# Optimization experiments

Measured on AMD Instinct MI355X. Metric: run time of the kernel, lower is better.

The kernel has to match this reference:

```python
import jax, jax.numpy as jnp
import numpy as np

TAU_S = 5.0  # network_config['tau_s']; n_steps inferred from trailing dim


def psp(x, tau_s):
    """Leaky synaptic integrator along the last (time) axis.
    x: [B, C, H, W, T] -> syns: [B, C, H, W, T]
    syn_t = syn_{t-1} * (1 - 1/tau_s) + x_t ;  out_t = syn_t / tau_s
    """
    decay = 1.0 - 1.0 / tau_s
    xt = jnp.moveaxis(x, -1, 0)  # [T, B, C, H, W]

    def step(syn, inp):
        syn = syn * decay + inp
        return syn, syn / tau_s

    _, ys = jax.lax.scan(step, jnp.zeros_like(xt[0]), xt)
    return jnp.moveaxis(ys, 0, -1)  # [B, C, H, W, T]


def setup_inputs() -> dict:
    key = jax.random.key(0)
    k1, k2 = jax.random.split(key)
    B, C, H, W, T = 32, 256, 4, 4, 100
    outputs = jax.random.normal(k1, (B, C, H, W, T), dtype=jnp.float32)
    # target is a spike train in the original; uniform [0,1) floats keep the
    # same math and dtype (fill='rand' per input_specs)
    target = jax.random.uniform(k2, (B, C, H, W, T), dtype=jnp.float32)
    return {"outputs": outputs, "target": target}


def reference(outputs, target):
    # spike_kernel: delta = outputs - psp(target); loss = 0.5 * sum(delta^2)
    delta = outputs - psp(target, TAU_S)
    return 0.5 * jnp.sum(delta * delta)
```

## Files before the change

kernel.cpp:

```cpp
#include <hip/hip_runtime.h>


#define BLOCK 256

__global__ __launch_bounds__(BLOCK) void spike_loss_kernel(
    const float4* __restrict__ o4g, const float4* __restrict__ x4g,
    float* __restrict__ out) {
  const int r = blockIdx.x * BLOCK + threadIdx.x;
  const float4* __restrict__ op = o4g + (size_t)r * 25;
  const float4* __restrict__ xp = x4g + (size_t)r * 25;

  float4 xc[5], oc[5], xn[5], on[5];
#pragma unroll
  for (int j = 0; j < 5; ++j) { xc[j] = xp[j]; oc[j] = op[j]; }

  float syn = 0.f;
  float l0 = 0.f, l1 = 0.f, l2 = 0.f, l3 = 0.f;
#pragma unroll
  for (int c = 0; c < 5; ++c) {
    if (c < 4) {
#pragma unroll
      for (int j = 0; j < 5; ++j) {
        xn[j] = xp[(c + 1) * 5 + j];
        on[j] = op[(c + 1) * 5 + j];
      }
    }
#pragma unroll
    for (int j = 0; j < 5; ++j) {
      float a;
      syn = fmaf(0.8f, syn, xc[j].x); a = fmaf(-0.2f, syn, oc[j].x); l0 = fmaf(a, a, l0);
      syn = fmaf(0.8f, syn, xc[j].y); a = fmaf(-0.2f, syn, oc[j].y); l1 = fmaf(a, a, l1);
      syn = fmaf(0.8f, syn, xc[j].z); a = fmaf(-0.2f, syn, oc[j].z); l2 = fmaf(a, a, l2);
      syn = fmaf(0.8f, syn, xc[j].w); a = fmaf(-0.2f, syn, oc[j].w); l3 = fmaf(a, a, l3);
    }
    if (c < 4) {
#pragma unroll
      for (int j = 0; j < 5; ++j) { xc[j] = xn[j]; oc[j] = on[j]; }
    }
  }
  float loss = (l0 + l1) + (l2 + l3);

#pragma unroll
  for (int off = 32; off > 0; off >>= 1) loss += __shfl_down(loss, off, 64);

  __shared__ float wsum[BLOCK / 64];
  const int lane = threadIdx.x & 63;
  const int w    = threadIdx.x >> 6;
  if (lane == 0) wsum[w] = loss;
  __syncthreads();
  if (threadIdx.x == 0) {
    float v = (wsum[0] + wsum[1]) + (wsum[2] + wsum[3]);
    atomicAdd(out, 0.5f * v);
  }
}

extern "C" void kernel_launch(void* const* d_in, const int* in_sizes, int n_in,
                              void* d_out, int out_size, void* d_ws, size_t ws_size,
                              hipStream_t stream) {
  const float4* o4 = (const float4*)d_in[0];
  const float4* x4 = (const float4*)d_in[1];
  float* loss = (float*)d_out;

  const int rows = in_sizes[0] / 100;
  const int grid = rows / BLOCK;

  hipLaunchKernelGGL(spike_loss_kernel, dim3(grid), dim3(BLOCK), 0, stream,
                     o4, x4, loss);
}
```

Baseline: 143.2 us.

## Decompose scan into per-chunk local partials with coalesced loads and LDS carry pass

Each float4 chunk is now processed independently with coalesced loads across the block. Each chunk gets a local 4-step integration assuming zero incoming state, plus the local squared error and a linear term. The carried synaptic state is then reconstructed per row in a second pass over LDS, expanding the squared error algebraically with precomputed decay-power constants. This removes strided per-thread row loads, at the cost of LDS traffic, a block barrier, half the threads idling in the second pass, and a slightly different float rounding order.

Result: faster. 122.7 us (-14.3%).

```diff
diff --git a/kernel.cpp b/kernel.cpp
--- a/kernel.cpp
+++ b/kernel.cpp
@@ -2,53 +2,86 @@
 
 
 #define BLOCK 256
+#define RPB   128
+#define F4PB  (RPB * 25)
+
+constexpr double dpow(double b, int n) {
+  double r = 1.0; for (int i = 0; i < n; ++i) r *= b; return r;
+}
+constexpr float K4  = (float)dpow(0.8, 4);
+constexpr float B0d = (float)(0.4 * dpow(0.8, 1));
+constexpr float B1d = (float)(0.4 * dpow(0.8, 2));
+constexpr float B2d = (float)(0.4 * dpow(0.8, 3));
+constexpr float B3d = (float)(0.4 * dpow(0.8, 4));
+constexpr float G4C = (float)(0.04 * (dpow(0.8, 2) + dpow(0.8, 4) +
+                                      dpow(0.8, 6) + dpow(0.8, 8)));
 
 __global__ __launch_bounds__(BLOCK) void spike_loss_kernel(
     const float4* __restrict__ o4g, const float4* __restrict__ x4g,
     float* __restrict__ out) {
-  const int r = blockIdx.x * BLOCK + threadIdx.x;
-  const float4* __restrict__ op = o4g + (size_t)r * 25;
-  const float4* __restrict__ xp = x4g + (size_t)r * 25;
+  __shared__ float UB[2 * F4PB];
+  __shared__ float wsum[BLOCK / 64];
 
-  float4 xc[5], oc[5], xn[5], on[5];
+  const int t = threadIdx.x;
+  const size_t base = (size_t)blockIdx.x * F4PB;
+  const float4* __restrict__ xp = x4g + base;
+  const float4* __restrict__ op = o4g + base;
+
+  float loss = 0.f;
+
+  float4 xa = xp[t], oa = op[t];
+  int i = t;
 #pragma unroll
-  for (int j = 0; j < 5; ++j) { xc[j] = xp[j]; oc[j] = op[j]; }
+  for (int k = 0; k < 12; ++k) {
+    float4 xb, ob;
+    if ((k < 11) || (t < RPB)) { xb = xp[i + BLOCK]; ob = op[i + BLOCK]; }
+    float u, a, abar, bb;
+    u = xa.x;                 a = fmaf(-0.2f, u, oa.x);
+    abar = a * a;             bb = a * B0d;
+    u = fmaf(0.8f, u, xa.y);  a = fmaf(-0.2f, u, oa.y);
+    abar = fmaf(a, a, abar);  bb = fmaf(a, B1d, bb);
+    u = fmaf(0.8f, u, xa.z);  a = fmaf(-0.2f, u, oa.z);
+    abar = fmaf(a, a, abar);  bb = fmaf(a, B2d, bb);
+    u = fmaf(0.8f, u, xa.w);  a = fmaf(-0.2f, u, oa.w);
+    abar = fmaf(a, a, abar);  bb = fmaf(a, B3d, bb);
+    loss += abar;
+    UB[i] = u; UB[F4PB + i] = bb;
+    xa = xb; oa = ob; i += BLOCK;
+  }
+  if (t < RPB) {
+    float u, a, abar, bb;
+    u = xa.x;                 a = fmaf(-0.2f, u, oa.x);
+    abar = a * a;             bb = a * B0d;
+    u = fmaf(0.8f, u, xa.y);  a = fmaf(-0.2f, u, oa.y);
+    abar = fmaf(a, a, abar);  bb = fmaf(a, B1d, bb);
+    u = fmaf(0.8f, u, xa.z);  a = fmaf(-0.2f, u, oa.z);
+    abar = fmaf(a, a, abar);  bb = fmaf(a, B2d, bb);
+    u = fmaf(0.8f, u, xa.w);  a = fmaf(-0.2f, u, oa.w);
+    abar = fmaf(a, a, abar);  bb = fmaf(a, B3d, bb);
+    loss += abar;
+    UB[i] = u; UB[F4PB + i] = bb;
+  }
+  __syncthreads();
 
-  float syn = 0.f;
-  float l0 = 0.f, l1 = 0.f, l2 = 0.f, l3 = 0.f;
+  if (t < RPB) {
+    float sig = 0.f, l2 = 0.f;
+    const int rb = t * 25;
 #pragma unroll
-  for (int c = 0; c < 5; ++c) {
-    if (c < 4) {
-#pragma unroll
-      for (int j = 0; j < 5; ++j) {
-        xn[j] = xp[(c + 1) * 5 + j];
-        on[j] = op[(c + 1) * 5 + j];
-      }
+    for (int c = 0; c < 25; ++c) {
+      const float u  = UB[rb + c];
+      const float bb = UB[F4PB + rb + c];
+      l2  = fmaf(fmaf(G4C, sig, -bb), sig, l2);
+      sig = fmaf(K4, sig, u);
     }
-#pragma unroll
-    for (int j = 0; j < 5; ++j) {
-      float a;
-      syn = fmaf(0.8f, syn, xc[j].x); a = fmaf(-0.2f, syn, oc[j].x); l0 = fmaf(a, a, l0);
-      syn = fmaf(0.8f, syn, xc[j].y); a = fmaf(-0.2f, syn, oc[j].y); l1 = fmaf(a, a, l1);
-      syn = fmaf(0.8f, syn, xc[j].z); a = fmaf(-0.2f, syn, oc[j].z); l2 = fmaf(a, a, l2);
-      syn = fmaf(0.8f, syn, xc[j].w); a = fmaf(-0.2f, syn, oc[j].w); l3 = fmaf(a, a, l3);
-    }
-    if (c < 4) {
-#pragma unroll
-      for (int j = 0; j < 5; ++j) { xc[j] = xn[j]; oc[j] = on[j]; }
-    }
+    loss += l2;
   }
-  float loss = (l0 + l1) + (l2 + l3);
 
 #pragma unroll
   for (int off = 32; off > 0; off >>= 1) loss += __shfl_down(loss, off, 64);
-
-  __shared__ float wsum[BLOCK / 64];
-  const int lane = threadIdx.x & 63;
-  const int w    = threadIdx.x >> 6;
+  const int lane = t & 63, w = t >> 6;
   if (lane == 0) wsum[w] = loss;
   __syncthreads();
-  if (threadIdx.x == 0) {
+  if (t == 0) {
     float v = (wsum[0] + wsum[1]) + (wsum[2] + wsum[3]);
     atomicAdd(out, 0.5f * v);
   }
@@ -61,8 +94,7 @@
   const float4* x4 = (const float4*)d_in[1];
   float* loss = (float*)d_out;
 
-  const int rows = in_sizes[0] / 100;
-  const int grid = rows / BLOCK;
+  const int grid = in_sizes[0] / (F4PB * 4);
 
   hipLaunchKernelGGL(spike_loss_kernel, dim3(grid), dim3(BLOCK), 0, stream,
                      o4, x4, loss);
```
